# Optimization experiments

Measured on AMD Instinct MI355X. Metric: run time of the kernel, lower is better.

## Reference

```python
import jax, jax.numpy as jnp
import numpy as np

N, C, NE = 65536, 128, 10
INV_SQ2 = float(1.0 / np.sqrt(2.0))   # path weight sqrt(ir_out.dim / n_paths) * w3j, 0e outputs
INV_SQ6 = float(1.0 / np.sqrt(6.0))   # sqrt(1/2) * 1/sqrt(3) for the 1o.1o->0e dot path


def _fcn(x, weights):
    # e3nn FullyConnectedNet: no biases, fan-in normalized, silu between layers
    h = x
    for i, W in enumerate(weights):
        h = (h @ W) * float(1.0 / np.sqrt(W.shape[0]))
        if i < len(weights) - 1:
            h = jax.nn.silu(h)
    return h


def setup_inputs() -> dict:
    key = jax.random.key(0)
    ks = jax.random.split(key, 24)
    elem = jax.random.randint(ks[0], (N,), 0, NE)
    return {
        'node_feats_s': jax.random.normal(ks[1], (N, C), jnp.float32),
        'node_feats_v': jax.random.normal(ks[2], (N, C, 3), jnp.float32),
        'sc': jax.random.normal(ks[3], (N, 4 * C), jnp.float32),
        'node_attrs': jax.nn.one_hot(elem, NE, dtype=jnp.float32),
        'magmom_node_inv_feats': jax.random.normal(ks[4], (N, 16), jnp.float32),
        'magmom_node_attrs': jax.random.normal(ks[5], (N, 4), jnp.float32),
        'magmom_lenghts': jax.random.uniform(ks[6], (N, 1), jnp.float32),
        'Ws': jax.random.normal(ks[7], (NE, 5, C), jnp.float32),
        'Wv': jax.random.normal(ks[8], (NE, 4, C), jnp.float32),
        'Wc1': jax.random.normal(ks[9], (16, 64), jnp.float32),
        'Wc2': jax.random.normal(ks[10], (64, 64), jnp.float32),
        'Wc3': jax.random.normal(ks[11], (64, 64), jnp.float32),
        'Wc4': jax.random.normal(ks[12], (64, 4 * C), jnp.float32),
        'Wb1': jax.random.normal(ks[13], (16, 64), jnp.float32),
        'Wb2': jax.random.normal(ks[14], (64, 64), jnp.float32),
        'Wb3': jax.random.normal(ks[15], (64, 64), jnp.float32),
        'Wb4': jax.random.normal(ks[16], (64, C), jnp.float32),
        'exp_scaling': jnp.full((1,), 5.0, jnp.float32),
        'Wl0': jax.random.normal(ks[17], (2 * C, C), jnp.float32),
        'Wl1': jax.random.normal(ks[18], (2 * C, C), jnp.float32),
        'Wo0': jax.random.normal(ks[19], (C, C), jnp.float32),
        'Wo1': jax.random.normal(ks[20], (C, C), jnp.float32),
    }


def reference(node_feats_s, node_feats_v, sc, node_attrs, magmom_node_inv_feats,
              magmom_node_attrs, magmom_lenghts, Ws, Wv, Wc1, Wc2, Wc3, Wc4,
              Wb1, Wb2, Wb3, Wb4, exp_scaling, Wl0, Wl1, Wo0, Wo1):
    s, v = node_feats_s, node_feats_v                     # [N,C], [N,C,3]
    # --- SymmetricContraction (correlation 3, l<=1): per-element weighted symmetric CG basis ---
    ws = jnp.einsum('ne,epc->npc', node_attrs, Ws)        # [N,5,C] element-selected weights
    wv = jnp.einsum('ne,epc->npc', node_attrs, Wv)        # [N,4,C]
    vv = jnp.sum(v * v, axis=-1)                          # [N,C] invariant |v|^2
    out_s = (ws[:, 0] * s + ws[:, 1] * (s * s) + ws[:, 2] * vv
             + ws[:, 3] * (s * s * s) + ws[:, 4] * (s * vv))
    gate = wv[:, 0] + wv[:, 1] * s + wv[:, 2] * (s * s) + wv[:, 3] * vv
    out_v = gate[..., None] * v                           # [N,C,3] all 1o basis terms are multiples of v
    # --- conv_tp weights from invariant magmom feats ---
    tp_w = _fcn(magmom_node_inv_feats, [Wc1, Wc2, Wc3, Wc4])   # [N,4C]
    w0, w1, w2, w3 = (tp_w[:, 0:C], tp_w[:, C:2 * C], tp_w[:, 2 * C:3 * C], tp_w[:, 3 * C:4 * C])
    y0 = magmom_node_attrs[:, 0:1]                        # 1x0e
    y1 = magmom_node_attrs[:, 1:4]                        # 1x1o
    # --- path-sparse TensorProduct (uvu, per-sample weights), 4 instructions ---
    m0 = INV_SQ2 * w0 * out_s * y0                                     # 0e x 0e -> 0e
    m1 = INV_SQ6 * w1 * jnp.einsum('nci,ni->nc', out_v, y1)           # 1o x 1o -> 0e
    m2 = INV_SQ2 * w2[..., None] * out_s[..., None] * y1[:, None, :]  # 0e x 1o -> 1o
    m3 = INV_SQ2 * w3[..., None] * out_v * y0[:, :, None]             # 1o x 0e -> 1o
    # --- one-body magmom basis added to the scalar channels ---
    ob = _fcn(magmom_node_inv_feats, [Wb1, Wb2, Wb3, Wb4])            # [N,C]
    m0 = m0 + (1.0 - jnp.exp(-exp_scaling * magmom_lenghts)) * ob
    # --- equivariant Linear(irreps_mid -> target) + Linear(target -> target) + sc ---
    scal = jnp.concatenate([m0, m1], axis=1)              # [N,2C] 0e block
    vecs = jnp.concatenate([m2, m3], axis=1)              # [N,2C,3] 1o block
    inv_2c = float(1.0 / np.sqrt(2 * C))
    inv_c = float(1.0 / np.sqrt(C))
    out0 = (scal @ Wl0) * inv_2c
    out1 = jnp.einsum('nci,co->noi', vecs, Wl1) * inv_2c
    o0 = (out_s @ Wo0) * inv_c
    o1 = jnp.einsum('nci,co->noi', out_v, Wo1) * inv_c
    msg0 = out0 + o0 + sc[:, :C]
    msg1 = (out1 + o1).reshape(-1, 3 * C) + sc[:, C:]
    return jnp.concatenate([msg0, msg1], axis=1)          # [N, 4C] = target_irreps.dim
```

## Files before the change

kernel.cpp:

```cpp
#include <hip/hip_runtime.h>

#define NNODES 65536
#define CC 128
#define NEL 10
#define BN 32
#define NT 256

#define INV_SQ2f 0.70710678118654752440f
#define INV_SQ6f 0.40824829046386301637f
#define INV_2Cf  0.0625f
#define INV_Cf   0.08838834764831845f
#define S16f 0.25f
#define S64f 0.125f

#define WS_FRAGS 312
#define WS_BYTES (WS_FRAGS * 1024)

typedef __attribute__((ext_vector_type(8))) short s16x8;
typedef __attribute__((ext_vector_type(4))) float f32x4;
#define MFMA16(a, b, c) __builtin_amdgcn_mfma_f32_16x16x32_bf16((a), (b), (c), 0, 0, 0)

union U8 { unsigned short u[8]; s16x8 s; };

__device__ __forceinline__ unsigned short bf16rne(float x) {
    unsigned int u = __float_as_uint(x);
    return (unsigned short)((u + 0x7FFFu + ((u >> 16) & 1u)) >> 16);
}
__device__ __forceinline__ float bf2f(unsigned short h) {
    return __uint_as_float(((unsigned int)h) << 16);
}
__device__ __forceinline__ unsigned int packbf(float a, float b) {
    return (unsigned int)bf16rne(a) | (((unsigned int)bf16rne(b)) << 16);
}
__device__ __forceinline__ float siluf(float x) {
    return x * (1.0f / (1.0f + __expf(-x)));
}

extern "C" __global__ void prep_frags(
    const float* __restrict__ WC1, const float* __restrict__ WC2,
    const float* __restrict__ WC3, const float* __restrict__ WB1,
    const float* __restrict__ WB2, const float* __restrict__ WB3,
    const float* __restrict__ WC4, const float* __restrict__ WB4,
    const float* __restrict__ WL0, const float* __restrict__ WO0,
    const float* __restrict__ WL1, const float* __restrict__ WO1,
    unsigned short* __restrict__ wsb)
{
    const int b = blockIdx.x;
    const int l = threadIdx.x;
    const float* W; int K, N, nKS, base; float sc;
    if      (b <  4) { W = WC1; K = 16;  N = 64;  nKS = 1; base = 0;   sc = S16f; }
    else if (b < 12) { W = WC2; K = 64;  N = 64;  nKS = 2; base = 4;   sc = S64f; }
    else if (b < 20) { W = WC3; K = 64;  N = 64;  nKS = 2; base = 12;  sc = S64f; }
    else if (b < 24) { W = WB1; K = 16;  N = 64;  nKS = 1; base = 20;  sc = S16f; }
    else if (b < 32) { W = WB2; K = 64;  N = 64;  nKS = 2; base = 24;  sc = S64f; }
    else if (b < 40) { W = WB3; K = 64;  N = 64;  nKS = 2; base = 32;  sc = S64f; }
    else if (b < 104){ W = WC4; K = 64;  N = 512; nKS = 2; base = 40;  sc = S64f; }
    else if (b < 120){ W = WB4; K = 64;  N = 128; nKS = 2; base = 104; sc = S64f; }
    else if (b < 184){ W = WL0; K = 256; N = 128; nKS = 8; base = 120; sc = INV_2Cf; }
    else if (b < 216){ W = WO0; K = 128; N = 128; nKS = 4; base = 184; sc = INV_Cf; }
    else if (b < 280){ W = WL1; K = 256; N = 128; nKS = 8; base = 216; sc = INV_2Cf; }
    else             { W = WO1; K = 128; N = 128; nKS = 4; base = 280; sc = INV_Cf; }
    const int f  = b - base;
    const int nt = f / nKS, ks = f % nKS;
    const int n  = nt * 16 + (l & 15);
    const int k0 = ks * 32 + (l >> 4) * 8;
    U8 v;
    #pragma unroll
    for (int j = 0; j < 8; ++j) {
        const int k = k0 + j;
        const float x = (k < K) ? W[(size_t)k * N + n] * sc : 0.0f;
        v.u[j] = bf16rne(x);
    }
    *(s16x8*)(wsb + (size_t)b * 512 + l * 8) = v.s;
}

__device__ __forceinline__ s16x8 ldB(const unsigned short* __restrict__ wsb, int fragidx, int lane) {
    return *(const s16x8*)(wsb + ((size_t)fragidx << 9) + lane * 8);
}
__device__ __forceinline__ s16x8 ldA136(const unsigned short* X, int row, int ks, int gq) {
    return *(const s16x8*)(X + row * 136 + ks * 32 + gq * 8);
}
__device__ __forceinline__ s16x8 ldA72(const unsigned short* X, int row, int ks, int gq) {
    return *(const s16x8*)(X + row * 72 + ks * 32 + gq * 8);
}

extern "C" __global__ void __launch_bounds__(NT)
epb_mfma(const float* __restrict__ Sin, const float* __restrict__ Vin,
         const float* __restrict__ SCp, const float* __restrict__ ATT,
         const float* __restrict__ INVF, const float* __restrict__ MNA,
         const float* __restrict__ MLEN, const float* __restrict__ WSp,
         const float* __restrict__ WVp, const float* __restrict__ ESC,
         const unsigned short* __restrict__ wsb, float* __restrict__ OUT)
{
    extern __shared__ char smem[];
    unsigned short* B1 = (unsigned short*)smem;
    unsigned short* B2 = B1 + 4352;
    unsigned short* B3 = B2 + 4352;
    unsigned short* B4 = B3 + 4352;
    unsigned short* B5 = B4 + 4352;
    unsigned short* B6 = B5 + 4352;
    float* y0f  = (float*)(smem + 6 * 8704);
    float* y1f  = y0f + 32;
    float* etf  = y1f + 96;
    int*   eidx = (int*)(etf + 32);

    const int tid  = threadIdx.x;
    const int n0   = blockIdx.x * BN;
    const int w    = tid >> 6;
    const int lane = tid & 63;
    const int cl   = lane & 15;
    const int gq   = lane >> 4;
    const f32x4 Z4 = {0.f, 0.f, 0.f, 0.f};

    U8 invu[2];
    #pragma unroll
    for (int rg = 0; rg < 2; ++rg) {
        if (gq < 2) {
            const float* ip = INVF + (size_t)(n0 + rg * 16 + cl) * 16 + gq * 8;
            #pragma unroll
            for (int j = 0; j < 8; ++j) invu[rg].u[j] = bf16rne(ip[j]);
        } else {
            #pragma unroll
            for (int j = 0; j < 8; ++j) invu[rg].u[j] = 0;
        }
    }

    if (tid < BN) {
        const int gn = n0 + tid;
        y0f[tid] = MNA[gn * 4 + 0];
        y1f[tid * 3 + 0] = MNA[gn * 4 + 1];
        y1f[tid * 3 + 1] = MNA[gn * 4 + 2];
        y1f[tid * 3 + 2] = MNA[gn * 4 + 3];
        etf[tid] = 1.0f - __expf(-ESC[0] * MLEN[gn]);
        int e = 0;
        #pragma unroll
        for (int k = 0; k < NEL; ++k)
            if (ATT[(size_t)gn * NEL + k] > 0.5f) e = k;
        eidx[tid] = e;
    }

    #pragma unroll
    for (int rg = 0; rg < 2; ++rg) {
        const f32x4 c = MFMA16(invu[rg].s, ldB(wsb, 0 + w, lane), Z4);
        const f32x4 b = MFMA16(invu[rg].s, ldB(wsb, 20 + w, lane), Z4);
        #pragma unroll
        for (int r = 0; r < 4; ++r) {
            const int rw = rg * 16 + gq * 4 + r;
            B1[rw * 72 + w * 16 + cl] = bf16rne(siluf(c[r]));
            B2[rw * 72 + w * 16 + cl] = bf16rne(siluf(b[r]));
        }
    }
    __syncthreads();

    {
        f32x4 c[2] = {Z4, Z4}, b[2] = {Z4, Z4};
        #pragma unroll
        for (int ks = 0; ks < 2; ++ks) {
            const s16x8 fc = ldB(wsb, 4 + w * 2 + ks, lane);
            const s16x8 fb = ldB(wsb, 24 + w * 2 + ks, lane);
            #pragma unroll
            for (int rg = 0; rg < 2; ++rg) {
                c[rg] = MFMA16(ldA72(B1, rg * 16 + cl, ks, gq), fc, c[rg]);
                b[rg] = MFMA16(ldA72(B2, rg * 16 + cl, ks, gq), fb, b[rg]);
            }
        }
        #pragma unroll
        for (int rg = 0; rg < 2; ++rg)
            #pragma unroll
            for (int r = 0; r < 4; ++r) {
                const int rw = rg * 16 + gq * 4 + r;
                B3[rw * 72 + w * 16 + cl] = bf16rne(siluf(c[rg][r]));
                B4[rw * 72 + w * 16 + cl] = bf16rne(siluf(b[rg][r]));
            }
    }
    __syncthreads();

    {
        f32x4 c[2] = {Z4, Z4}, b[2] = {Z4, Z4};
        #pragma unroll
        for (int ks = 0; ks < 2; ++ks) {
            const s16x8 fc = ldB(wsb, 12 + w * 2 + ks, lane);
            const s16x8 fb = ldB(wsb, 32 + w * 2 + ks, lane);
            #pragma unroll
            for (int rg = 0; rg < 2; ++rg) {
                c[rg] = MFMA16(ldA72(B3, rg * 16 + cl, ks, gq), fc, c[rg]);
                b[rg] = MFMA16(ldA72(B4, rg * 16 + cl, ks, gq), fb, b[rg]);
            }
        }
        #pragma unroll
        for (int rg = 0; rg < 2; ++rg)
            #pragma unroll
            for (int r = 0; r < 4; ++r) {
                const int rw = rg * 16 + gq * 4 + r;
                B1[rw * 72 + w * 16 + cl] = bf16rne(siluf(c[rg][r]));
                B2[rw * 72 + w * 16 + cl] = bf16rne(siluf(b[rg][r]));
            }
    }
    __syncthreads();

    s16x8 h3c[2][2], h3b[2][2];
    #pragma unroll
    for (int rg = 0; rg < 2; ++rg)
        #pragma unroll
        for (int ks = 0; ks < 2; ++ks) {
            h3c[rg][ks] = ldA72(B1, rg * 16 + cl, ks, gq);
            h3b[rg][ks] = ldA72(B2, rg * 16 + cl, ks, gq);
        }
    __syncthreads();

    f32x4 obacc[2][2], wc0[2][2], wc1[2][2];
    #pragma unroll
    for (int tc = 0; tc < 2; ++tc) {
        const int T = w * 2 + tc;
        const s16x8 f0 = ldB(wsb, 104 + T * 2 + 0, lane);
        const s16x8 f1 = ldB(wsb, 104 + T * 2 + 1, lane);
        const s16x8 a0 = ldB(wsb, 40 + (0 * 8 + T) * 2 + 0, lane);
        const s16x8 a1 = ldB(wsb, 40 + (0 * 8 + T) * 2 + 1, lane);
        const s16x8 b0 = ldB(wsb, 40 + (1 * 8 + T) * 2 + 0, lane);
        const s16x8 b1 = ldB(wsb, 40 + (1 * 8 + T) * 2 + 1, lane);
        #pragma unroll
        for (int rg = 0; rg < 2; ++rg) {
            obacc[rg][tc] = MFMA16(h3b[rg][1], f1, MFMA16(h3b[rg][0], f0, Z4));
            wc0[rg][tc]   = MFMA16(h3c[rg][1], a1, MFMA16(h3c[rg][0], a0, Z4));
            wc1[rg][tc]   = MFMA16(h3c[rg][1], b1, MFMA16(h3c[rg][0], b0, Z4));
        }
    }

    unsigned int vpack[3][8];
    {
        const int row = tid >> 3;
        const int c0  = (tid & 7) << 4;
        const size_t gn = (size_t)(n0 + row);
        const int e = eidx[row];
        const float y10 = y1f[row * 3], y11 = y1f[row * 3 + 1], y12 = y1f[row * 3 + 2];
        const float* sp  = Sin + gn * CC + c0;
        const float* vp  = Vin + (gn * CC + c0) * 3;
        const float* wsp = WSp + ((size_t)e * 5) * CC + c0;
        const float* wvp = WVp + ((size_t)e * 4) * CC + c0;
        unsigned int* B1d = (unsigned int*)B1;
        unsigned int* B2d = (unsigned int*)B2;
        unsigned int* B3d = (unsigned int*)B3;
        const int dbase = row * 68 + (c0 >> 1);
        #pragma unroll
        for (int jp = 0; jp < 8; ++jp) {
            const int c = 2 * jp;
            const float2 s2 = *(const float2*)(sp + c);
            const float2 va = *(const float2*)(vp + 3 * c);
            const float2 vb = *(const float2*)(vp + 3 * c + 2);
            const float2 vc = *(const float2*)(vp + 3 * c + 4);
            vpack[0][jp] = packbf(va.x, vb.y);
            vpack[1][jp] = packbf(va.y, vc.x);
            vpack[2][jp] = packbf(vb.x, vc.y);
            const float vv0 = va.x * va.x + va.y * va.y + vb.x * vb.x;
            const float vv1 = vb.y * vb.y + vc.x * vc.x + vc.y * vc.y;
            const float vy0 = va.x * y10 + va.y * y11 + vb.x * y12;
            const float vy1 = vb.y * y10 + vc.x * y11 + vc.y * y12;
            const float2 p0 = *(const float2*)(wsp + 0 * CC + c);
            const float2 p1 = *(const float2*)(wsp + 1 * CC + c);
            const float2 p2 = *(const float2*)(wsp + 2 * CC + c);
            const float2 p3 = *(const float2*)(wsp + 3 * CC + c);
            const float2 p4 = *(const float2*)(wsp + 4 * CC + c);
            const float2 q0 = *(const float2*)(wvp + 0 * CC + c);
            const float2 q1 = *(const float2*)(wvp + 1 * CC + c);
            const float2 q2 = *(const float2*)(wvp + 2 * CC + c);
            const float2 q3 = *(const float2*)(wvp + 3 * CC + c);
            const float s0 = s2.x, s1 = s2.y;
            const float ss0 = s0 * s0, ss1 = s1 * s1;
            const float os0 = p0.x * s0 + p1.x * ss0 + p2.x * vv0 + p3.x * (ss0 * s0) + p4.x * (s0 * vv0);
            const float os1 = p0.y * s1 + p1.y * ss1 + p2.y * vv1 + p3.y * (ss1 * s1) + p4.y * (s1 * vv1);
            const float gt0 = q0.x + q1.x * s0 + q2.x * ss0 + q3.x * vv0;
            const float gt1 = q0.y + q1.y * s1 + q2.y * ss1 + q3.y * vv1;
            B1d[dbase + jp] = packbf(os0, os1);
            B2d[dbase + jp] = packbf(gt0, gt1);
            B3d[dbase + jp] = packbf(vy0, vy1);
        }
    }
    __syncthreads();

    #pragma unroll
    for (int rg = 0; rg < 2; ++rg)
        #pragma unroll
        for (int tc = 0; tc < 2; ++tc)
            #pragma unroll
            for (int r = 0; r < 4; ++r) {
                const int rw = rg * 16 + gq * 4 + r;
                const int col = (w * 2 + tc) * 16 + cl;
                const float gt = bf2f(B2[rw * 136 + col]);
                const float vy = bf2f(B3[rw * 136 + col]);
                B3[rw * 136 + col] = bf16rne(INV_SQ6f * wc1[rg][tc][r] * gt * vy);
                const float os = bf2f(B1[rw * 136 + col]);
                const float m0 = INV_SQ2f * wc0[rg][tc][r] * os * y0f[rw] + etf[rw] * obacc[rg][tc][r];
                B4[rw * 136 + col] = bf16rne(m0);
            }
    __syncthreads();

    {
        f32x4 acc[2][2] = {{Z4, Z4}, {Z4, Z4}};
        #pragma unroll
        for (int ks = 0; ks < 12; ++ks) {
            const unsigned short* Xa = (ks < 4) ? B4 : (ks < 8) ? B3 : B1;
            s16x8 a[2];
            #pragma unroll
            for (int rg = 0; rg < 2; ++rg) a[rg] = ldA136(Xa, rg * 16 + cl, ks & 3, gq);
            #pragma unroll
            for (int tc = 0; tc < 2; ++tc) {
                const int T = w * 2 + tc;
                const int fi = (ks < 8) ? (120 + T * 8 + ks) : (184 + T * 4 + (ks - 8));
                const s16x8 bfrag = ldB(wsb, fi, lane);
                #pragma unroll
                for (int rg = 0; rg < 2; ++rg)
                    acc[rg][tc] = MFMA16(a[rg], bfrag, acc[rg][tc]);
            }
        }
        #pragma unroll
        for (int rg = 0; rg < 2; ++rg)
            #pragma unroll
            for (int tc = 0; tc < 2; ++tc)
                #pragma unroll
                for (int r = 0; r < 4; ++r) {
                    const int rw = rg * 16 + gq * 4 + r;
                    const size_t o = (size_t)(n0 + rw) * 512 + (w * 2 + tc) * 16 + cl;
                    OUT[o] = acc[rg][tc][r] + SCp[o];
                }
    }
    __syncthreads();

    {
        f32x4 wc2[2][2], wc3[2][2];
        #pragma unroll
        for (int tc = 0; tc < 2; ++tc) {
            const int T = w * 2 + tc;
            const s16x8 a0 = ldB(wsb, 40 + (2 * 8 + T) * 2 + 0, lane);
            const s16x8 a1 = ldB(wsb, 40 + (2 * 8 + T) * 2 + 1, lane);
            const s16x8 b0 = ldB(wsb, 40 + (3 * 8 + T) * 2 + 0, lane);
            const s16x8 b1 = ldB(wsb, 40 + (3 * 8 + T) * 2 + 1, lane);
            #pragma unroll
            for (int rg = 0; rg < 2; ++rg) {
                wc2[rg][tc] = MFMA16(h3c[rg][1], a1, MFMA16(h3c[rg][0], a0, Z4));
                wc3[rg][tc] = MFMA16(h3c[rg][1], b1, MFMA16(h3c[rg][0], b0, Z4));
            }
        }
        #pragma unroll
        for (int rg = 0; rg < 2; ++rg)
            #pragma unroll
            for (int tc = 0; tc < 2; ++tc)
                #pragma unroll
                for (int r = 0; r < 4; ++r) {
                    const int rw = rg * 16 + gq * 4 + r;
                    const int col = (w * 2 + tc) * 16 + cl;
                    B1[rw * 136 + col] = bf16rne(INV_SQ2f * wc2[rg][tc][r] * bf2f(B1[rw * 136 + col]));
                    const float gt = bf2f(B2[rw * 136 + col]);
                    B4[rw * 136 + col] = bf16rne(INV_SQ2f * wc3[rg][tc][r] * gt * y0f[rw]);
                }
    }
    __syncthreads();

    f32x4 tacc[2][2] = {{Z4, Z4}, {Z4, Z4}};
    #pragma unroll
    for (int ks = 0; ks < 4; ++ks) {
        s16x8 a[2];
        #pragma unroll
        for (int rg = 0; rg < 2; ++rg) a[rg] = ldA136(B1, rg * 16 + cl, ks, gq);
        #pragma unroll
        for (int tc = 0; tc < 2; ++tc) {
            const s16x8 bfrag = ldB(wsb, 216 + (w * 2 + tc) * 8 + ks, lane);
            #pragma unroll
            for (int rg = 0; rg < 2; ++rg)
                tacc[rg][tc] = MFMA16(a[rg], bfrag, tacc[rg][tc]);
        }
    }
    __syncthreads();

    f32x4 acc3[3][2][2];

#define STAGE_I(i, DSTB, DSTG)                                                  \
    {                                                                           \
        const int dbase = (tid >> 3) * 68 + (tid & 7) * 8;                      \
        const unsigned int* bD = (const unsigned int*)B4;                       \
        const unsigned int* gD = (const unsigned int*)B2;                       \
        unsigned int* o1 = (unsigned int*)(DSTB);                               \
        unsigned int* o3 = (unsigned int*)(DSTG);                               \
        _Pragma("unroll")                                                       \
        for (int jp = 0; jp < 8; ++jp) {                                        \
            const unsigned int bd = bD[dbase + jp];                             \
            const unsigned int gd = gD[dbase + jp];                             \
            const float v0 = bf2f((unsigned short)(vpack[i][jp] & 0xffff));     \
            const float v1 = bf2f((unsigned short)(vpack[i][jp] >> 16));        \
            o1[dbase + jp] = packbf(bf2f((unsigned short)(bd & 0xffff)) * v0,   \
                                    bf2f((unsigned short)(bd >> 16)) * v1);     \
            o3[dbase + jp] = packbf(bf2f((unsigned short)(gd & 0xffff)) * v0,   \
                                    bf2f((unsigned short)(gd >> 16)) * v1);     \
        }                                                                       \
    }

#define GEMM_I(i, SRCB, SRCG)                                                   \
    {                                                                           \
        _Pragma("unroll")                                                       \
        for (int rg = 0; rg < 2; ++rg)                                          \
            _Pragma("unroll")                                                   \
            for (int tc = 0; tc < 2; ++tc) acc3[i][rg][tc] = Z4;                \
        _Pragma("unroll")                                                       \
        for (int ks = 0; ks < 4; ++ks) {                                        \
            s16x8 a1[2], a3[2];                                                 \
            _Pragma("unroll")                                                   \
            for (int rg = 0; rg < 2; ++rg) {                                    \
                a1[rg] = ldA136((SRCB), rg * 16 + cl, ks, gq);                  \
                a3[rg] = ldA136((SRCG), rg * 16 + cl, ks, gq);                  \
            }                                                                   \
            _Pragma("unroll")                                                   \
            for (int tc = 0; tc < 2; ++tc) {                                    \
                const int T = w * 2 + tc;                                       \
                const s16x8 fb = ldB(wsb, 216 + T * 8 + 4 + ks, lane);          \
                const s16x8 fg = ldB(wsb, 280 + T * 4 + ks, lane);              \
                _Pragma("unroll")                                               \
                for (int rg = 0; rg < 2; ++rg) {                                \
                    acc3[i][rg][tc] = MFMA16(a1[rg], fb, acc3[i][rg][tc]);      \
                    acc3[i][rg][tc] = MFMA16(a3[rg], fg, acc3[i][rg][tc]);      \
                }                                                               \
            }                                                                   \
        }                                                                       \
    }

    STAGE_I(0, B1, B3)
    __syncthreads();
    GEMM_I(0, B1, B3)
    STAGE_I(1, B5, B6)
    __syncthreads();
    GEMM_I(1, B5, B6)
    STAGE_I(2, B1, B3)
    __syncthreads();
    GEMM_I(2, B1, B3)

    #pragma unroll
    for (int rg = 0; rg < 2; ++rg)
        #pragma unroll
        for (int tc = 0; tc < 2; ++tc)
            #pragma unroll
            for (int r = 0; r < 4; ++r) {
                const int rw = rg * 16 + gq * 4 + r;
                const int col = (w * 2 + tc) * 16 + cl;
                const size_t o = (size_t)(n0 + rw) * 512 + 128 + (size_t)col * 3;
                const float tv = tacc[rg][tc][r];
                OUT[o + 0] = acc3[0][rg][tc][r] + tv * y1f[rw * 3 + 0] + SCp[o + 0];
                OUT[o + 1] = acc3[1][rg][tc][r] + tv * y1f[rw * 3 + 1] + SCp[o + 1];
                OUT[o + 2] = acc3[2][rg][tc][r] + tv * y1f[rw * 3 + 2] + SCp[o + 2];
            }
#undef STAGE_I
#undef GEMM_I
}

extern "C" void kernel_launch(void* const* d_in, const int* in_sizes, int n_in,
                              void* d_out, int out_size, void* d_ws, size_t ws_size,
                              hipStream_t stream)
{
    (void)in_sizes; (void)n_in; (void)out_size; (void)ws_size;
    const float* Sin  = (const float*)d_in[0];
    const float* Vin  = (const float*)d_in[1];
    const float* SCp  = (const float*)d_in[2];
    const float* ATT  = (const float*)d_in[3];
    const float* INVF = (const float*)d_in[4];
    const float* MNA  = (const float*)d_in[5];
    const float* MLEN = (const float*)d_in[6];
    const float* WSp  = (const float*)d_in[7];
    const float* WVp  = (const float*)d_in[8];
    const float* WC1  = (const float*)d_in[9];
    const float* WC2  = (const float*)d_in[10];
    const float* WC3  = (const float*)d_in[11];
    const float* WC4  = (const float*)d_in[12];
    const float* WB1  = (const float*)d_in[13];
    const float* WB2  = (const float*)d_in[14];
    const float* WB3  = (const float*)d_in[15];
    const float* WB4  = (const float*)d_in[16];
    const float* ESC  = (const float*)d_in[17];
    const float* WL0  = (const float*)d_in[18];
    const float* WL1  = (const float*)d_in[19];
    const float* WO0  = (const float*)d_in[20];
    const float* WO1  = (const float*)d_in[21];
    float* OUT = (float*)d_out;

    unsigned short* wsb = (unsigned short*)d_ws;
    hipLaunchKernelGGL(prep_frags, dim3(WS_FRAGS), dim3(64), 0, stream,
                       WC1, WC2, WC3, WB1, WB2, WB3, WC4, WB4,
                       WL0, WO0, WL1, WO1, wsb);
    const size_t shbytes = (size_t)(6 * 8704 + 768);
    hipLaunchKernelGGL(epb_mfma, dim3(NNODES / BN), dim3(NT), shbytes, stream,
                       Sin, Vin, SCp, ATT, INVF, MNA, MLEN, WSp, WVp, ESC,
                       wsb, OUT);
}
```

Baseline: 163.6 us.

## Stream weight-gen chunks through spare LDS buffers and drop extra barriers

Writes the hidden activations to separate LDS buffers (B5/B6) so the barrier after loading them can go. The four weight-generation MFMA chunks now run one at a time, each consumed right away, which cuts live accumulator registers. The separate pass for the 1o-path scalings and the tacc GEMM is folded into the scalar-output phase, removing two barriers. Element index and y1 are now read directly from global one-hot attributes and magmom attrs per thread, which adds redundant global loads and a 10-way compare per thread.

```diff
diff --git a/kernel.cpp b/kernel.cpp
--- a/kernel.cpp
+++ b/kernel.cpp
@@ -192,8 +192,8 @@
             #pragma unroll
             for (int r = 0; r < 4; ++r) {
                 const int rw = rg * 16 + gq * 4 + r;
-                B1[rw * 72 + w * 16 + cl] = bf16rne(siluf(c[rg][r]));
-                B2[rw * 72 + w * 16 + cl] = bf16rne(siluf(b[rg][r]));
+                B5[rw * 72 + w * 16 + cl] = bf16rne(siluf(c[rg][r]));
+                B6[rw * 72 + w * 16 + cl] = bf16rne(siluf(b[rg][r]));
             }
     }
     __syncthreads();
@@ -203,27 +203,18 @@
     for (int rg = 0; rg < 2; ++rg)
         #pragma unroll
         for (int ks = 0; ks < 2; ++ks) {
-            h3c[rg][ks] = ldA72(B1, rg * 16 + cl, ks, gq);
-            h3b[rg][ks] = ldA72(B2, rg * 16 + cl, ks, gq);
-        }
-    __syncthreads();
-
-    f32x4 obacc[2][2], wc0[2][2], wc1[2][2];
+            h3c[rg][ks] = ldA72(B5, rg * 16 + cl, ks, gq);
+            h3b[rg][ks] = ldA72(B6, rg * 16 + cl, ks, gq);
+        }
+    f32x4 obacc[2][2];
     #pragma unroll
     for (int tc = 0; tc < 2; ++tc) {
         const int T = w * 2 + tc;
         const s16x8 f0 = ldB(wsb, 104 + T * 2 + 0, lane);
         const s16x8 f1 = ldB(wsb, 104 + T * 2 + 1, lane);
-        const s16x8 a0 = ldB(wsb, 40 + (0 * 8 + T) * 2 + 0, lane);
-        const s16x8 a1 = ldB(wsb, 40 + (0 * 8 + T) * 2 + 1, lane);
-        const s16x8 b0 = ldB(wsb, 40 + (1 * 8 + T) * 2 + 0, lane);
-        const s16x8 b1 = ldB(wsb, 40 + (1 * 8 + T) * 2 + 1, lane);
-        #pragma unroll
-        for (int rg = 0; rg < 2; ++rg) {
+        #pragma unroll
+        for (int rg = 0; rg < 2; ++rg)
             obacc[rg][tc] = MFMA16(h3b[rg][1], f1, MFMA16(h3b[rg][0], f0, Z4));
-            wc0[rg][tc]   = MFMA16(h3c[rg][1], a1, MFMA16(h3c[rg][0], a0, Z4));
-            wc1[rg][tc]   = MFMA16(h3c[rg][1], b1, MFMA16(h3c[rg][0], b0, Z4));
-        }
     }
 
     unsigned int vpack[3][8];
@@ -231,8 +222,12 @@
         const int row = tid >> 3;
         const int c0  = (tid & 7) << 4;
         const size_t gn = (size_t)(n0 + row);
-        const int e = eidx[row];
-        const float y10 = y1f[row * 3], y11 = y1f[row * 3 + 1], y12 = y1f[row * 3 + 2];
+        const float4 mna = *(const float4*)(MNA + gn * 4);
+        const float y10 = mna.y, y11 = mna.z, y12 = mna.w;
+        int e = 0;
+        #pragma unroll
+        for (int k = 0; k < NEL; ++k)
+            if (ATT[gn * NEL + k] > 0.5f) e = k;
         const float* sp  = Sin + gn * CC + c0;
         const float* vp  = Vin + (gn * CC + c0) * 3;
         const float* wsp = WSp + ((size_t)e * 5) * CC + c0;
@@ -277,23 +272,74 @@
     }
     __syncthreads();
 
-    #pragma unroll
-    for (int rg = 0; rg < 2; ++rg)
-        #pragma unroll
-        for (int tc = 0; tc < 2; ++tc)
-            #pragma unroll
-            for (int r = 0; r < 4; ++r) {
-                const int rw = rg * 16 + gq * 4 + r;
-                const int col = (w * 2 + tc) * 16 + cl;
-                const float gt = bf2f(B2[rw * 136 + col]);
-                const float vy = bf2f(B3[rw * 136 + col]);
-                B3[rw * 136 + col] = bf16rne(INV_SQ6f * wc1[rg][tc][r] * gt * vy);
-                const float os = bf2f(B1[rw * 136 + col]);
-                const float m0 = INV_SQ2f * wc0[rg][tc][r] * os * y0f[rw] + etf[rw] * obacc[rg][tc][r];
-                B4[rw * 136 + col] = bf16rne(m0);
-            }
-    __syncthreads();
-
+#define WCHUNK(q, wc)                                                          \
+    {                                                                          \
+        _Pragma("unroll")                                                      \
+        for (int tc = 0; tc < 2; ++tc) {                                       \
+            const int T = w * 2 + tc;                                          \
+            const s16x8 f0 = ldB(wsb, 40 + ((q) * 8 + T) * 2 + 0, lane);       \
+            const s16x8 f1 = ldB(wsb, 40 + ((q) * 8 + T) * 2 + 1, lane);       \
+            _Pragma("unroll")                                                  \
+            for (int rg = 0; rg < 2; ++rg)                                     \
+                wc[rg][tc] = MFMA16(h3c[rg][1], f1, MFMA16(h3c[rg][0], f0, Z4)); \
+        }                                                                      \
+    }
+    {
+        f32x4 wc[2][2];
+        WCHUNK(0, wc)
+        #pragma unroll
+        for (int rg = 0; rg < 2; ++rg)
+            #pragma unroll
+            for (int tc = 0; tc < 2; ++tc)
+                #pragma unroll
+                for (int r = 0; r < 4; ++r) {
+                    const int rw = rg * 16 + gq * 4 + r;
+                    const int col = (w * 2 + tc) * 16 + cl;
+                    const float os = bf2f(B1[rw * 136 + col]);
+                    B4[rw * 136 + col] = bf16rne(INV_SQ2f * wc[rg][tc][r] * os * y0f[rw]
+                                                 + etf[rw] * obacc[rg][tc][r]);
+                }
+        WCHUNK(1, wc)
+        #pragma unroll
+        for (int rg = 0; rg < 2; ++rg)
+            #pragma unroll
+            for (int tc = 0; tc < 2; ++tc)
+                #pragma unroll
+                for (int r = 0; r < 4; ++r) {
+                    const int rw = rg * 16 + gq * 4 + r;
+                    const int col = (w * 2 + tc) * 16 + cl;
+                    const float gt = bf2f(B2[rw * 136 + col]);
+                    const float vy = bf2f(B3[rw * 136 + col]);
+                    B3[rw * 136 + col] = bf16rne(INV_SQ6f * wc[rg][tc][r] * gt * vy);
+                }
+        WCHUNK(2, wc)
+        #pragma unroll
+        for (int rg = 0; rg < 2; ++rg)
+            #pragma unroll
+            for (int tc = 0; tc < 2; ++tc)
+                #pragma unroll
+                for (int r = 0; r < 4; ++r) {
+                    const int rw = rg * 16 + gq * 4 + r;
+                    const int col = (w * 2 + tc) * 16 + cl;
+                    B6[rw * 136 + col] = bf16rne(INV_SQ2f * wc[rg][tc][r] * bf2f(B1[rw * 136 + col]));
+                }
+        WCHUNK(3, wc)
+        #pragma unroll
+        for (int rg = 0; rg < 2; ++rg)
+            #pragma unroll
+            for (int tc = 0; tc < 2; ++tc)
+                #pragma unroll
+                for (int r = 0; r < 4; ++r) {
+                    const int rw = rg * 16 + gq * 4 + r;
+                    const int col = (w * 2 + tc) * 16 + cl;
+                    const float gt = bf2f(B2[rw * 136 + col]);
+                    B5[rw * 136 + col] = bf16rne(INV_SQ2f * wc[rg][tc][r] * gt * y0f[rw]);
+                }
+    }
+#undef WCHUNK
+    __syncthreads();
+
+    f32x4 tacc[2][2] = {{Z4, Z4}, {Z4, Z4}};
     {
         f32x4 acc[2][2] = {{Z4, Z4}, {Z4, Z4}};
         #pragma unroll
@@ -310,6 +356,19 @@
                 #pragma unroll
                 for (int rg = 0; rg < 2; ++rg)
                     acc[rg][tc] = MFMA16(a[rg], bfrag, acc[rg][tc]);
+            }
+        }
+        #pragma unroll
+        for (int ks = 0; ks < 4; ++ks) {
+            s16x8 a[2];
+            #pragma unroll
+            for (int rg = 0; rg < 2; ++rg) a[rg] = ldA136(B6, rg * 16 + cl, ks, gq);
+            #pragma unroll
+            for (int tc = 0; tc < 2; ++tc) {
+                const s16x8 bfrag = ldB(wsb, 216 + (w * 2 + tc) * 8 + ks, lane);
+                #pragma unroll
+                for (int rg = 0; rg < 2; ++rg)
+                    tacc[rg][tc] = MFMA16(a[rg], bfrag, tacc[rg][tc]);
             }
         }
         #pragma unroll
@@ -325,58 +384,12 @@
     }
     __syncthreads();
 
-    {
-        f32x4 wc2[2][2], wc3[2][2];
-        #pragma unroll
-        for (int tc = 0; tc < 2; ++tc) {
-            const int T = w * 2 + tc;
-            const s16x8 a0 = ldB(wsb, 40 + (2 * 8 + T) * 2 + 0, lane);
-            const s16x8 a1 = ldB(wsb, 40 + (2 * 8 + T) * 2 + 1, lane);
-            const s16x8 b0 = ldB(wsb, 40 + (3 * 8 + T) * 2 + 0, lane);
-            const s16x8 b1 = ldB(wsb, 40 + (3 * 8 + T) * 2 + 1, lane);
-            #pragma unroll
-            for (int rg = 0; rg < 2; ++rg) {
-                wc2[rg][tc] = MFMA16(h3c[rg][1], a1, MFMA16(h3c[rg][0], a0, Z4));
-                wc3[rg][tc] = MFMA16(h3c[rg][1], b1, MFMA16(h3c[rg][0], b0, Z4));
-            }
-        }
-        #pragma unroll
-        for (int rg = 0; rg < 2; ++rg)
-            #pragma unroll
-            for (int tc = 0; tc < 2; ++tc)
-                #pragma unroll
-                for (int r = 0; r < 4; ++r) {
-                    const int rw = rg * 16 + gq * 4 + r;
-                    const int col = (w * 2 + tc) * 16 + cl;
-                    B1[rw * 136 + col] = bf16rne(INV_SQ2f * wc2[rg][tc][r] * bf2f(B1[rw * 136 + col]));
-                    const float gt = bf2f(B2[rw * 136 + col]);
-                    B4[rw * 136 + col] = bf16rne(INV_SQ2f * wc3[rg][tc][r] * gt * y0f[rw]);
-                }
-    }
-    __syncthreads();
-
-    f32x4 tacc[2][2] = {{Z4, Z4}, {Z4, Z4}};
-    #pragma unroll
-    for (int ks = 0; ks < 4; ++ks) {
-        s16x8 a[2];
-        #pragma unroll
-        for (int rg = 0; rg < 2; ++rg) a[rg] = ldA136(B1, rg * 16 + cl, ks, gq);
-        #pragma unroll
-        for (int tc = 0; tc < 2; ++tc) {
-            const s16x8 bfrag = ldB(wsb, 216 + (w * 2 + tc) * 8 + ks, lane);
-            #pragma unroll
-            for (int rg = 0; rg < 2; ++rg)
-                tacc[rg][tc] = MFMA16(a[rg], bfrag, tacc[rg][tc]);
-        }
-    }
-    __syncthreads();
-
     f32x4 acc3[3][2][2];
 
 #define STAGE_I(i, DSTB, DSTG)                                                  \
     {                                                                           \
         const int dbase = (tid >> 3) * 68 + (tid & 7) * 8;                      \
-        const unsigned int* bD = (const unsigned int*)B4;                       \
+        const unsigned int* bD = (const unsigned int*)B5;                       \
         const unsigned int* gD = (const unsigned int*)B2;                       \
         unsigned int* o1 = (unsigned int*)(DSTB);                               \
         unsigned int* o3 = (unsigned int*)(DSTG);                               \
@@ -424,9 +437,9 @@
     STAGE_I(0, B1, B3)
     __syncthreads();
     GEMM_I(0, B1, B3)
-    STAGE_I(1, B5, B6)
-    __syncthreads();
-    GEMM_I(1, B5, B6)
+    STAGE_I(1, B4, B6)
+    __syncthreads();
+    GEMM_I(1, B4, B6)
     STAGE_I(2, B1, B3)
     __syncthreads();
     GEMM_I(2, B1, B3)
```

Result: no change. 166.4 us (+1.7%).
